# Kernel tuning notes

Hardware: AMD Instinct MI355X
Metric: run time of the kernel (lower is better)

Reference implementation:

```python
import jax, jax.numpy as jnp
import numpy as np

N_NODES = 50000
N_EDGES = 800000
IN_DIM = 128
HID = 64
N_LAYERS = 3


def setup_inputs() -> dict:
    key = jax.random.key(0)
    ks = jax.random.split(key, 12)
    x = jax.random.normal(ks[0], (N_NODES, IN_DIM), dtype=jnp.float32)
    edge_index = jax.random.randint(ks[1], (2, N_EDGES), 0, N_NODES, dtype=jnp.int64)
    s = 0.05
    Wp = jax.random.normal(ks[2], (IN_DIM, HID), dtype=jnp.float32) * s
    bp = jax.random.normal(ks[3], (HID,), dtype=jnp.float32) * s
    # per-layer EdgeConv MLP params, stacked over layers
    W1 = jax.random.normal(ks[4], (N_LAYERS, 2 * HID, HID), dtype=jnp.float32) * s
    b1 = jax.random.normal(ks[5], (N_LAYERS, HID), dtype=jnp.float32) * s
    W2 = jax.random.normal(ks[6], (N_LAYERS, HID, HID), dtype=jnp.float32) * s
    b2 = jax.random.normal(ks[7], (N_LAYERS, HID), dtype=jnp.float32) * s
    Wo = jax.random.normal(ks[8], (HID, 1), dtype=jnp.float32) * s
    bo = jax.random.normal(ks[9], (1,), dtype=jnp.float32) * s
    return {"x": x, "edge_index": edge_index, "Wp": Wp, "bp": bp,
            "W1": W1, "b1": b1, "W2": W2, "b2": b2, "Wo": Wo, "bo": bo}


def _edge_conv(h, src, dst, W1, b1, W2, b2):
    # PyG EdgeConv: message = MLP(cat[x_i, x_j - x_i]), aggr = max over incoming edges
    xi = h[dst]                       # [E, H] center (target) features
    xj = h[src]                       # [E, H] neighbor (source) features
    e = jnp.concatenate([xi, xj - xi], axis=-1)   # [E, 2H]
    m = jnp.maximum(e @ W1 + b1, 0.0) @ W2 + b2   # [E, H]
    agg = jax.ops.segment_max(m, dst, num_segments=N_NODES)  # [N, H]
    # nodes with no incoming edges get 0 (PyG scatter-max fill value)
    return jnp.where(jnp.isfinite(agg), agg, 0.0)


def reference(x, edge_index, Wp, bp, W1, b1, W2, b2, Wo, bo):
    src, dst = edge_index[0], edge_index[1]
    h = x @ Wp + bp                   # input projection [N, H]
    for l in range(N_LAYERS):
        residual = h
        h = _edge_conv(h, src, dst, W1[l], b1[l], W2[l], b2[l])
        h = jnp.maximum(h, 0.0)       # relu; dropout is identity in eval
        h = h + residual
    return (h @ Wo + bo)[:, 0]        # squeeze(-1) -> [N]
```

## Files before the change

kernel.cpp:

```cpp
#include <hip/hip_runtime.h>

#define NN 50000
#define IN_DIM 128
#define HID 64
#define NLAYERS 3
#define NB 1563
#define CH 128
#define NPART 8
#define BPP 196
#define PQ_BLOCKS 782

typedef __attribute__((ext_vector_type(8))) _Float16 f16x8;
typedef __attribute__((ext_vector_type(2))) _Float16 f16x2;
typedef __attribute__((ext_vector_type(4))) float f32x4;

__device__ __forceinline__ unsigned pkh(float a, float b) {
    return __builtin_bit_cast(unsigned, __builtin_amdgcn_cvt_pkrtz(a, b));
}
__device__ __forceinline__ unsigned short f2h(float f) {
    f16x2 v = __builtin_bit_cast(f16x2, __builtin_amdgcn_cvt_pkrtz(f, 0.f));
    return __builtin_bit_cast(short2, v).x;
}

__device__ __forceinline__ unsigned addrelu2(unsigned q, unsigned p) {
    f16x2 qq = __builtin_bit_cast(f16x2, q);
    f16x2 pp = __builtin_bit_cast(f16x2, p);
    f16x2 s = qq + pp;
    f16x2 z = {(_Float16)0.f, (_Float16)0.f};
    f16x2 r = __builtin_elementwise_max(s, z);
    return __builtin_bit_cast(unsigned, r);
}


__global__ void __launch_bounds__(256) k_hist(const int* __restrict__ dst,
                                              int* __restrict__ cntc, int E, int CE) {
    __shared__ int lh[NB];
    int g = blockIdx.x;
    for (int i = threadIdx.x; i < NB; i += 256) lh[i] = 0;
    __syncthreads();
    int e0 = g * CE, e1 = min(E, e0 + CE);
    for (int e = e0 + threadIdx.x; e < e1; e += 256) atomicAdd(&lh[dst[e] >> 5], 1);
    __syncthreads();
    for (int i = threadIdx.x; i < NB; i += 256) cntc[g * NB + i] = lh[i];
}

__global__ void k_base(const int* __restrict__ cntc, int* __restrict__ basec,
                       int* __restrict__ bincnt) {
    int b = blockIdx.x * 256 + threadIdx.x;
    if (b < NB) {
        int run = 0;
        for (int g = 0; g < CH; g++) {
            basec[g * NB + b] = run;
            run += cntc[g * NB + b];
        }
        bincnt[b] = run;
    }
}

__global__ void k_binscan(const int* __restrict__ bincnt, int* __restrict__ binoff) {
    __shared__ int s[256];
    int t = threadIdx.x;
    int carry = 0;
    for (int c0 = 0; c0 < NB; c0 += 256) {
        int v = (c0 + t < NB) ? bincnt[c0 + t] : 0;
        s[t] = v;
        __syncthreads();
        for (int d = 1; d < 256; d <<= 1) {
            int a = (t >= d) ? s[t - d] : 0;
            __syncthreads();
            s[t] += a;
            __syncthreads();
        }
        if (c0 + t < NB) binoff[c0 + t] = carry + s[t] - v;
        carry += s[255];
        __syncthreads();
    }
}

__global__ void __launch_bounds__(256) k_scatter(
    const int* __restrict__ src, const int* __restrict__ dst,
    const int* __restrict__ basec, const int* __restrict__ binoff,
    unsigned* __restrict__ bscratch, int E, int CE) {
    __shared__ int cur[BPP];
    int p = blockIdx.x & (NPART - 1);
    int g = blockIdx.x >> 3;
    int blo = p * BPP, bhi = min(NB, blo + BPP);
    for (int i = threadIdx.x; i < bhi - blo; i += 256) {
        int b = blo + i;
        cur[i] = binoff[b] + basec[g * NB + b];
    }
    __syncthreads();
    int e0 = g * CE, e1 = min(E, e0 + CE);
    for (int e = e0 + threadIdx.x; e < e1; e += 256) {
        int d = dst[e];
        int bin = d >> 5;
        if (bin >= blo && bin < bhi) {
            int pos = atomicAdd(&cur[bin - blo], 1);
            bscratch[pos] = ((unsigned)(d & 31) << 16) | (unsigned)src[e];
        }
    }
}

__global__ void __launch_bounds__(256) k_binsort(
    const unsigned* __restrict__ bscratch, const int* __restrict__ bincnt,
    const int* __restrict__ binoff, unsigned short* __restrict__ csr,
    int2* __restrict__ meta) {
    __shared__ unsigned entries[1024];
    __shared__ unsigned short sorted[1024];
    __shared__ int cnt[32];
    int bin = blockIdx.x, t = threadIdx.x;
    int n = bincnt[bin], boff = binoff[bin];
    for (int i = t; i < n; i += 256) entries[i] = bscratch[boff + i];
    if (t < 32) cnt[t] = 0;
    __syncthreads();
    for (int i = t; i < n; i += 256) atomicAdd(&cnt[entries[i] >> 16], 1);
    __syncthreads();
    if (t < 32) {
        int c = cnt[t];
        int s = c;
#pragma unroll
        for (int d = 1; d < 32; d <<= 1) {
            int o = __shfl_up(s, d, 64);
            if (t >= d) s += o;
        }
        int node = bin * 32 + t;
        if (node < NN) meta[node] = make_int2(boff + s - c, c);
        cnt[t] = s - c;
    }
    __syncthreads();
    for (int i = t; i < n; i += 256) {
        unsigned e = entries[i];
        int p = atomicAdd(&cnt[e >> 16], 1);
        sorted[p] = (unsigned short)(e & 0xffffu);
    }
    __syncthreads();
    for (int i = t; i < n; i += 256) csr[boff + i] = sorted[i];
}


__global__ void __launch_bounds__(256) k_projpq(
    const float* __restrict__ x, const float* __restrict__ Wp,
    const float* __restrict__ bp, const float* __restrict__ W1,
    const float* __restrict__ b1, float* __restrict__ h,
    unsigned short* __restrict__ P, unsigned short* __restrict__ Qb) {
    __shared__ float hs[4][16][66];
    int lane = threadIdx.x & 63, wave = threadIdx.x >> 6;
    int col = lane & 15, quad = lane >> 4;
    int node0 = (blockIdx.x * 4 + wave) * 16;
    if (node0 >= NN) return;

    f16x8 bw[4][4];
#pragma unroll
    for (int t = 0; t < 4; t++)
#pragma unroll
        for (int kc = 0; kc < 4; kc++) {
            uint4 u;
#pragma unroll
            for (int jp = 0; jp < 4; jp++) {
                int k0 = kc * 32 + quad * 8 + jp * 2;
                ((unsigned*)&u)[jp] = pkh(Wp[k0 * HID + t * 16 + col],
                                          Wp[(k0 + 1) * HID + t * 16 + col]);
            }
            bw[t][kc] = __builtin_bit_cast(f16x8, u);
        }
    const float4* xr = (const float4*)(x + (size_t)(node0 + col) * IN_DIM);
    f16x8 ax[4];
#pragma unroll
    for (int kc = 0; kc < 4; kc++) {
        float4 f0 = xr[kc * 8 + quad * 2], f1 = xr[kc * 8 + quad * 2 + 1];
        uint4 u;
        u.x = pkh(f0.x, f0.y); u.y = pkh(f0.z, f0.w);
        u.z = pkh(f1.x, f1.y); u.w = pkh(f1.z, f1.w);
        ax[kc] = __builtin_bit_cast(f16x8, u);
    }
#pragma unroll
    for (int t = 0; t < 4; t++) {
        f32x4 c = (f32x4)(0.f);
#pragma unroll
        for (int kc = 0; kc < 4; kc++)
            c = __builtin_amdgcn_mfma_f32_16x16x32_f16(ax[kc], bw[t][kc], c, 0, 0, 0);
        float bv = bp[t * 16 + col];
#pragma unroll
        for (int r = 0; r < 4; r++) {
            float hv = c[r] + bv;
            int row = quad * 4 + r;
            h[(size_t)(node0 + row) * HID + t * 16 + col] = hv;
            hs[wave][row][t * 16 + col] = hv;
        }
    }

    f16x8 bfr[8][2];
#pragma unroll
    for (int t = 0; t < 8; t++)
#pragma unroll
        for (int hf = 0; hf < 2; hf++) {
            uint4 u;
#pragma unroll
            for (int jp = 0; jp < 4; jp++) {
                int k0 = hf * 32 + quad * 8 + jp * 2;
                float w0, w1v;
                if (t < 4) {
                    int n = t * 16 + col;
                    w0  = W1[k0 * HID + n] - W1[(HID + k0) * HID + n];
                    w1v = W1[(k0 + 1) * HID + n] - W1[(HID + k0 + 1) * HID + n];
                } else {
                    int n = (t - 4) * 16 + col;
                    w0  = W1[(HID + k0) * HID + n];
                    w1v = W1[(HID + k0 + 1) * HID + n];
                }
                ((unsigned*)&u)[jp] = pkh(w0, w1v);
            }
            bfr[t][hf] = __builtin_bit_cast(f16x8, u);
        }
    const float* hl = &hs[wave][col][0];
    uint4 au, bu;
    {
        float2 e0 = *(const float2*)(hl + quad * 8);
        float2 e1 = *(const float2*)(hl + quad * 8 + 2);
        float2 e2 = *(const float2*)(hl + quad * 8 + 4);
        float2 e3 = *(const float2*)(hl + quad * 8 + 6);
        au.x = pkh(e0.x, e0.y); au.y = pkh(e1.x, e1.y);
        au.z = pkh(e2.x, e2.y); au.w = pkh(e3.x, e3.y);
        float2 f0 = *(const float2*)(hl + 32 + quad * 8);
        float2 f1 = *(const float2*)(hl + 32 + quad * 8 + 2);
        float2 f2 = *(const float2*)(hl + 32 + quad * 8 + 4);
        float2 f3 = *(const float2*)(hl + 32 + quad * 8 + 6);
        bu.x = pkh(f0.x, f0.y); bu.y = pkh(f1.x, f1.y);
        bu.z = pkh(f2.x, f2.y); bu.w = pkh(f3.x, f3.y);
    }
    f16x8 a0 = __builtin_bit_cast(f16x8, au);
    f16x8 a1 = __builtin_bit_cast(f16x8, bu);
#pragma unroll
    for (int t = 0; t < 8; t++) {
        f32x4 c = __builtin_amdgcn_mfma_f32_16x16x32_f16(a0, bfr[t][0], (f32x4)(0.f), 0, 0, 0);
        c = __builtin_amdgcn_mfma_f32_16x16x32_f16(a1, bfr[t][1], c, 0, 0, 0);
        if (t < 4) {
            float bv = b1[t * 16 + col];
#pragma unroll
            for (int r = 0; r < 4; r++)
                P[(size_t)(node0 + quad * 4 + r) * HID + t * 16 + col] = f2h(c[r] + bv);
        } else {
#pragma unroll
            for (int r = 0; r < 4; r++)
                Qb[(size_t)(node0 + quad * 4 + r) * HID + (t - 4) * 16 + col] = f2h(c[r]);
        }
    }
}

__global__ void __launch_bounds__(256) k_pq_mfma(
    const float* __restrict__ h, const float* __restrict__ W1,
    const float* __restrict__ b1, unsigned short* __restrict__ P,
    unsigned short* __restrict__ Qb, int layer) {
    int lane = threadIdx.x & 63, wave = threadIdx.x >> 6;
    int col = lane & 15, quad = lane >> 4;
    int node0 = (blockIdx.x * 4 + wave) * 16;
    if (node0 >= NN) return;
    const float* W1l = W1 + layer * 2 * HID * HID;

    f16x8 bfr[8][2];
#pragma unroll
    for (int t = 0; t < 8; t++)
#pragma unroll
        for (int hf = 0; hf < 2; hf++) {
            uint4 u;
#pragma unroll
            for (int jp = 0; jp < 4; jp++) {
                int k0 = hf * 32 + quad * 8 + jp * 2;
                float w0, w1v;
                if (t < 4) {
                    int n = t * 16 + col;
                    w0  = W1l[k0 * HID + n] - W1l[(HID + k0) * HID + n];
                    w1v = W1l[(k0 + 1) * HID + n] - W1l[(HID + k0 + 1) * HID + n];
                } else {
                    int n = (t - 4) * 16 + col;
                    w0  = W1l[(HID + k0) * HID + n];
                    w1v = W1l[(HID + k0 + 1) * HID + n];
                }
                ((unsigned*)&u)[jp] = pkh(w0, w1v);
            }
            bfr[t][hf] = __builtin_bit_cast(f16x8, u);
        }

    const float* hrow = h + (size_t)(node0 + col) * HID;
    float4 ha0 = *(const float4*)(hrow + quad * 8);
    float4 ha1 = *(const float4*)(hrow + quad * 8 + 4);
    float4 hb0 = *(const float4*)(hrow + 32 + quad * 8);
    float4 hb1 = *(const float4*)(hrow + 32 + quad * 8 + 4);
    uint4 au, bu;
    au.x = pkh(ha0.x, ha0.y); au.y = pkh(ha0.z, ha0.w);
    au.z = pkh(ha1.x, ha1.y); au.w = pkh(ha1.z, ha1.w);
    bu.x = pkh(hb0.x, hb0.y); bu.y = pkh(hb0.z, hb0.w);
    bu.z = pkh(hb1.x, hb1.y); bu.w = pkh(hb1.z, hb1.w);
    f16x8 a0 = __builtin_bit_cast(f16x8, au);
    f16x8 a1 = __builtin_bit_cast(f16x8, bu);

#pragma unroll
    for (int t = 0; t < 8; t++) {
        f32x4 c = __builtin_amdgcn_mfma_f32_16x16x32_f16(a0, bfr[t][0], (f32x4)(0.f), 0, 0, 0);
        c = __builtin_amdgcn_mfma_f32_16x16x32_f16(a1, bfr[t][1], c, 0, 0, 0);
        if (t < 4) {
            float bv = b1[layer * HID + t * 16 + col];
#pragma unroll
            for (int r = 0; r < 4; r++)
                P[(size_t)(node0 + quad * 4 + r) * HID + t * 16 + col] = f2h(c[r] + bv);
        } else {
#pragma unroll
            for (int r = 0; r < 4; r++)
                Qb[(size_t)(node0 + quad * 4 + r) * HID + (t - 4) * 16 + col] = f2h(c[r]);
        }
    }
}

__global__ void __launch_bounds__(256) k_edge(
    const unsigned short* __restrict__ P, const unsigned short* __restrict__ Qb,
    const float* __restrict__ W2, const float* __restrict__ b2,
    const int2* __restrict__ meta, const unsigned short* __restrict__ csr,
    float* __restrict__ h, int layer, int nw,
    int fin, const float* __restrict__ Wo, const float* __restrict__ bo,
    float* __restrict__ outp) {
    __shared__ uint4 qstage[4][16][9];
    int lane = threadIdx.x & 63;
    int col = lane & 15, quad = lane >> 4;
    int wave = threadIdx.x >> 6;
    int rrow = lane >> 3, sseg = lane & 7;
    int wid = (blockIdx.x * blockDim.x + threadIdx.x) >> 6;

    const float* W2l = W2 + layer * HID * HID;
    f16x8 bfr[4][2];
#pragma unroll
    for (int t = 0; t < 4; t++)
#pragma unroll
        for (int hf = 0; hf < 2; hf++) {
            uint4 u;
#pragma unroll
            for (int jp = 0; jp < 4; jp++) {
                int k0 = hf * 32 + quad * 8 + jp * 2;
                ((unsigned*)&u)[jp] = pkh(W2l[k0 * HID + t * 16 + col],
                                          W2l[(k0 + 1) * HID + t * 16 + col]);
            }
            bfr[t][hf] = __builtin_bit_cast(f16x8, u);
        }
    float b2v = b2[layer * HID + lane];
    float wov = fin ? Wo[lane] : 0.f;

    for (int node = wid; node < NN; node += nw) {
        int2 md = meta[node];
        int start = __builtin_amdgcn_readfirstlane(md.x);
        int cnt   = __builtin_amdgcn_readfirstlane(md.y);
        float res = h[(size_t)node * HID + lane];
        float outv = 0.f;
        if (cnt > 0) {
            const uint4* prow = (const uint4*)(P + (size_t)node * HID);
            uint4 p0 = prow[quad];
            uint4 p1 = prow[4 + quad];
            f32x4 mx[4];
#pragma unroll
            for (int t = 0; t < 4; t++) mx[t] = (f32x4)(-3.4e38f);
            int nbatch = (cnt + 15) >> 4;
            uint4 v1, v2;
            {
                int e1 = rrow, e2 = 8 + rrow;
                int s1 = csr[start + (e1 < cnt ? e1 : 0)];
                int s2 = csr[start + (e2 < cnt ? e2 : 0)];
                v1 = ((const uint4*)(Qb + (size_t)s1 * HID))[sseg];
                v2 = ((const uint4*)(Qb + (size_t)s2 * HID))[sseg];
            }
            for (int b = 0; b < nbatch; b++) {
                qstage[wave][rrow][sseg] = v1;
                qstage[wave][8 + rrow][sseg] = v2;
                if (b + 1 < nbatch) {
                    int b0 = (b + 1) * 16;
                    int e1 = b0 + rrow, e2 = b0 + 8 + rrow;
                    int s1 = csr[start + (e1 < cnt ? e1 : b0)];
                    int s2 = csr[start + (e2 < cnt ? e2 : b0)];
                    v1 = ((const uint4*)(Qb + (size_t)s1 * HID))[sseg];
                    v2 = ((const uint4*)(Qb + (size_t)s2 * HID))[sseg];
                }
                uint4 q0 = qstage[wave][col][quad];
                uint4 q1 = qstage[wave][col][4 + quad];
                uint4 a0u, a1u;
                a0u.x = addrelu2(q0.x, p0.x);
                a0u.y = addrelu2(q0.y, p0.y);
                a0u.z = addrelu2(q0.z, p0.z);
                a0u.w = addrelu2(q0.w, p0.w);
                a1u.x = addrelu2(q1.x, p1.x);
                a1u.y = addrelu2(q1.y, p1.y);
                a1u.z = addrelu2(q1.z, p1.z);
                a1u.w = addrelu2(q1.w, p1.w);
                f16x8 a0 = __builtin_bit_cast(f16x8, a0u);
                f16x8 a1 = __builtin_bit_cast(f16x8, a1u);
#pragma unroll
                for (int t = 0; t < 4; t++) {
                    f32x4 c = __builtin_amdgcn_mfma_f32_16x16x32_f16(
                        a0, bfr[t][0], (f32x4)(0.f), 0, 0, 0);
                    c = __builtin_amdgcn_mfma_f32_16x16x32_f16(
                        a1, bfr[t][1], c, 0, 0, 0);
#pragma unroll
                    for (int r = 0; r < 4; r++)
                        mx[t][r] = fmaxf(mx[t][r], c[r]);
                }
            }
            float v[4];
#pragma unroll
            for (int t = 0; t < 4; t++) {
                v[t] = fmaxf(fmaxf(mx[t][0], mx[t][1]), fmaxf(mx[t][2], mx[t][3]));
                v[t] = fmaxf(v[t], __shfl_xor(v[t], 16, 64));
                v[t] = fmaxf(v[t], __shfl_xor(v[t], 32, 64));
            }
            float vs = quad == 0 ? v[0] : quad == 1 ? v[1] : quad == 2 ? v[2] : v[3];
            outv = fmaxf(vs + b2v, 0.f);
        }
        float hv = outv + res;
        h[(size_t)node * HID + lane] = hv;
        if (fin) {
            float v = hv * wov;
#pragma unroll
            for (int m = 32; m >= 1; m >>= 1) v += __shfl_xor(v, m, 64);
            if (lane == 0) outp[node] = v + bo[0];
        }
    }
}

extern "C" void kernel_launch(void* const* d_in, const int* in_sizes, int n_in,
                              void* d_out, int out_size, void* d_ws, size_t ws_size,
                              hipStream_t stream) {
    const float* x  = (const float*)d_in[0];
    const int*   ei = (const int*)d_in[1];
    const float* Wp = (const float*)d_in[2];
    const float* bp = (const float*)d_in[3];
    const float* W1 = (const float*)d_in[4];
    const float* b1 = (const float*)d_in[5];
    const float* W2 = (const float*)d_in[6];
    const float* b2 = (const float*)d_in[7];
    const float* Wo = (const float*)d_in[8];
    const float* bo = (const float*)d_in[9];
    float* out = (float*)d_out;

    const int E = in_sizes[1] / 2;
    const int N = NN;
    const int* srcp = ei;
    const int* dstp = ei + E;

    float* h  = (float*)d_ws;
    unsigned short* Pb = (unsigned short*)(h + (size_t)N * HID);
    unsigned short* Qb = Pb + (size_t)N * HID;
    int* cntc   = (int*)(Qb + (size_t)N * HID);
    int* basec  = cntc + CH * NB;
    int* bincnt = basec + CH * NB;
    int* binoff = bincnt + NB;
    int2* meta  = (int2*)(binoff + NB);
    unsigned* bscratch = (unsigned*)(meta + N);
    unsigned short* csr = (unsigned short*)(bscratch + E);

    const int CE = (E + CH - 1) / CH;

    k_hist<<<CH, 256, 0, stream>>>(dstp, cntc, E, CE);
    k_base<<<(NB + 255) / 256, 256, 0, stream>>>(cntc, basec, bincnt);
    k_binscan<<<1, 256, 0, stream>>>(bincnt, binoff);
    k_scatter<<<CH * NPART, 256, 0, stream>>>(srcp, dstp, basec, binoff, bscratch, E, CE);
    k_binsort<<<NB, 256, 0, stream>>>(bscratch, bincnt, binoff, csr, meta);

    k_projpq<<<PQ_BLOCKS, 256, 0, stream>>>(x, Wp, bp, W1, b1, h, Pb, Qb);

    const int EDGE_BLOCKS = 2048;
    const int NW = EDGE_BLOCKS * 256 / 64;
    for (int l = 0; l < NLAYERS; l++) {
        if (l > 0)
            k_pq_mfma<<<PQ_BLOCKS, 256, 0, stream>>>(h, W1, b1, Pb, Qb, l);
        k_edge<<<EDGE_BLOCKS, 256, 0, stream>>>(Pb, Qb, W2, b2, meta, csr, h, l, NW,
                                                l == NLAYERS - 1 ? 1 : 0, Wo, bo, out);
    }
}
```

Before: 288.1 us.

## Store hidden state in fp16, gather Q rows directly, prefetch next node metadata

The hidden state h moves from fp32 to fp16 storage, which halves its read and write traffic and drops the per-load packing in k_pq_mfma. The edge kernel stops staging Q rows through shared memory: each lane loads its own neighbor's Q row straight into MFMA operand layout and prefetches the next batch. It also prefetches the next node's meta entry and residual value across the node loop. Keeping the residual in fp16 adds rounding error that accumulates over the three layers, and the direct per-lane gathers may coalesce less well than the old staged loads.

```diff
diff --git a/kernel.cpp b/kernel.cpp
--- a/kernel.cpp
+++ b/kernel.cpp
@@ -20,6 +20,9 @@
 __device__ __forceinline__ unsigned short f2h(float f) {
     f16x2 v = __builtin_bit_cast(f16x2, __builtin_amdgcn_cvt_pkrtz(f, 0.f));
     return __builtin_bit_cast(short2, v).x;
+}
+__device__ __forceinline__ float h2f(unsigned short u) {
+    return (float)__builtin_bit_cast(_Float16, u);
 }
 
 __device__ __forceinline__ unsigned addrelu2(unsigned q, unsigned p) {
@@ -141,7 +144,7 @@
 __global__ void __launch_bounds__(256) k_projpq(
     const float* __restrict__ x, const float* __restrict__ Wp,
     const float* __restrict__ bp, const float* __restrict__ W1,
-    const float* __restrict__ b1, float* __restrict__ h,
+    const float* __restrict__ b1, unsigned short* __restrict__ h,
     unsigned short* __restrict__ P, unsigned short* __restrict__ Qb) {
     __shared__ float hs[4][16][66];
     int lane = threadIdx.x & 63, wave = threadIdx.x >> 6;
@@ -184,7 +187,7 @@
         for (int r = 0; r < 4; r++) {
             float hv = c[r] + bv;
             int row = quad * 4 + r;
-            h[(size_t)(node0 + row) * HID + t * 16 + col] = hv;
+            h[(size_t)(node0 + row) * HID + t * 16 + col] = f2h(hv);
             hs[wave][row][t * 16 + col] = hv;
         }
     }
@@ -248,7 +251,7 @@
 }
 
 __global__ void __launch_bounds__(256) k_pq_mfma(
-    const float* __restrict__ h, const float* __restrict__ W1,
+    const unsigned short* __restrict__ h, const float* __restrict__ W1,
     const float* __restrict__ b1, unsigned short* __restrict__ P,
     unsigned short* __restrict__ Qb, int layer) {
     int lane = threadIdx.x & 63, wave = threadIdx.x >> 6;
@@ -281,16 +284,9 @@
             bfr[t][hf] = __builtin_bit_cast(f16x8, u);
         }
 
-    const float* hrow = h + (size_t)(node0 + col) * HID;
-    float4 ha0 = *(const float4*)(hrow + quad * 8);
-    float4 ha1 = *(const float4*)(hrow + quad * 8 + 4);
-    float4 hb0 = *(const float4*)(hrow + 32 + quad * 8);
-    float4 hb1 = *(const float4*)(hrow + 32 + quad * 8 + 4);
-    uint4 au, bu;
-    au.x = pkh(ha0.x, ha0.y); au.y = pkh(ha0.z, ha0.w);
-    au.z = pkh(ha1.x, ha1.y); au.w = pkh(ha1.z, ha1.w);
-    bu.x = pkh(hb0.x, hb0.y); bu.y = pkh(hb0.z, hb0.w);
-    bu.z = pkh(hb1.x, hb1.y); bu.w = pkh(hb1.z, hb1.w);
+    const uint4* hrow = (const uint4*)(h + (size_t)(node0 + col) * HID);
+    uint4 au = hrow[quad];
+    uint4 bu = hrow[4 + quad];
     f16x8 a0 = __builtin_bit_cast(f16x8, au);
     f16x8 a1 = __builtin_bit_cast(f16x8, bu);
 
@@ -315,14 +311,11 @@
     const unsigned short* __restrict__ P, const unsigned short* __restrict__ Qb,
     const float* __restrict__ W2, const float* __restrict__ b2,
     const int2* __restrict__ meta, const unsigned short* __restrict__ csr,
-    float* __restrict__ h, int layer, int nw,
+    unsigned short* __restrict__ h, int layer, int nw,
     int fin, const float* __restrict__ Wo, const float* __restrict__ bo,
     float* __restrict__ outp) {
-    __shared__ uint4 qstage[4][16][9];
     int lane = threadIdx.x & 63;
     int col = lane & 15, quad = lane >> 4;
-    int wave = threadIdx.x >> 6;
-    int rrow = lane >> 3, sseg = lane & 7;
     int wid = (blockIdx.x * blockDim.x + threadIdx.x) >> 6;
 
     const float* W2l = W2 + layer * HID * HID;
@@ -343,11 +336,18 @@
     float b2v = b2[layer * HID + lane];
     float wov = fin ? Wo[lane] : 0.f;
 
+    if (wid >= NN) return;
+    int2 md = meta[wid];
+    unsigned short hres = h[(size_t)wid * HID + lane];
+
     for (int node = wid; node < NN; node += nw) {
-        int2 md = meta[node];
+        int pf = (node + nw < NN) ? node + nw : node;
+        int2 nmd = meta[pf];
+        unsigned short nhres = h[(size_t)pf * HID + lane];
+
         int start = __builtin_amdgcn_readfirstlane(md.x);
         int cnt   = __builtin_amdgcn_readfirstlane(md.y);
-        float res = h[(size_t)node * HID + lane];
+        float res = h2f(hres);
         float outv = 0.f;
         if (cnt > 0) {
             const uint4* prow = (const uint4*)(P + (size_t)node * HID);
@@ -357,27 +357,19 @@
 #pragma unroll
             for (int t = 0; t < 4; t++) mx[t] = (f32x4)(-3.4e38f);
             int nbatch = (cnt + 15) >> 4;
-            uint4 v1, v2;
-            {
-                int e1 = rrow, e2 = 8 + rrow;
-                int s1 = csr[start + (e1 < cnt ? e1 : 0)];
-                int s2 = csr[start + (e2 < cnt ? e2 : 0)];
-                v1 = ((const uint4*)(Qb + (size_t)s1 * HID))[sseg];
-                v2 = ((const uint4*)(Qb + (size_t)s2 * HID))[sseg];
-            }
+            int s = csr[start + (col < cnt ? col : 0)];
+            const uint4* qr = (const uint4*)(Qb + (size_t)s * HID);
+            uint4 q0 = qr[quad], q1 = qr[4 + quad];
             for (int b = 0; b < nbatch; b++) {
-                qstage[wave][rrow][sseg] = v1;
-                qstage[wave][8 + rrow][sseg] = v2;
+                uint4 nq0, nq1;
                 if (b + 1 < nbatch) {
                     int b0 = (b + 1) * 16;
-                    int e1 = b0 + rrow, e2 = b0 + 8 + rrow;
-                    int s1 = csr[start + (e1 < cnt ? e1 : b0)];
-                    int s2 = csr[start + (e2 < cnt ? e2 : b0)];
-                    v1 = ((const uint4*)(Qb + (size_t)s1 * HID))[sseg];
-                    v2 = ((const uint4*)(Qb + (size_t)s2 * HID))[sseg];
+                    int idx = b0 + col;
+                    int s2 = csr[start + (idx < cnt ? idx : b0)];
+                    const uint4* qr2 = (const uint4*)(Qb + (size_t)s2 * HID);
+                    nq0 = qr2[quad];
+                    nq1 = qr2[4 + quad];
                 }
-                uint4 q0 = qstage[wave][col][quad];
-                uint4 q1 = qstage[wave][col][4 + quad];
                 uint4 a0u, a1u;
                 a0u.x = addrelu2(q0.x, p0.x);
                 a0u.y = addrelu2(q0.y, p0.y);
@@ -399,6 +391,8 @@
                     for (int r = 0; r < 4; r++)
                         mx[t][r] = fmaxf(mx[t][r], c[r]);
                 }
+                q0 = nq0;
+                q1 = nq1;
             }
             float v[4];
 #pragma unroll
@@ -411,13 +405,15 @@
             outv = fmaxf(vs + b2v, 0.f);
         }
         float hv = outv + res;
-        h[(size_t)node * HID + lane] = hv;
+        h[(size_t)node * HID + lane] = f2h(hv);
         if (fin) {
             float v = hv * wov;
 #pragma unroll
             for (int m = 32; m >= 1; m >>= 1) v += __shfl_xor(v, m, 64);
             if (lane == 0) outp[node] = v + bo[0];
         }
+        md = nmd;
+        hres = nhres;
     }
 }
 
@@ -441,8 +437,8 @@
     const int* srcp = ei;
     const int* dstp = ei + E;
 
-    float* h  = (float*)d_ws;
-    unsigned short* Pb = (unsigned short*)(h + (size_t)N * HID);
+    unsigned short* h  = (unsigned short*)d_ws;
+    unsigned short* Pb = h + (size_t)N * HID;
     unsigned short* Qb = Pb + (size_t)N * HID;
     int* cntc   = (int*)(Qb + (size_t)N * HID);
     int* basec  = cntc + CH * NB;
```

Measured after the change: 292.2 us. Within noise of the previous version (+1.4%).
